# Kernel optimization log

Measured on AMD Instinct MI355X. Metric: run time of the kernel, lower is better.

## Reference

```python
import jax, jax.numpy as jnp
import numpy as np

N_HEADS, D_MODEL, DK, DV = 16, 1024, 64, 64
B, S = 4, 2048
NEG = -1000000000.0


def setup_inputs() -> dict:
    key = jax.random.key(0)
    ks = jax.random.split(key, 10)
    inp = {
        "q": jax.random.normal(ks[0], (B, S, D_MODEL), jnp.float32),
        "k": jax.random.normal(ks[1], (B, S, D_MODEL), jnp.float32),
        "v": jax.random.normal(ks[2], (B, S, D_MODEL), jnp.float32),
        "padding_mask": jax.random.randint(ks[3], (B, 1, S), 0, 2, jnp.int32),
        # linear params (torch Linear: y = x @ W.T + b); store as [in, out]
        "w_q": jax.random.normal(ks[4], (D_MODEL, N_HEADS * DK), jnp.float32) * 0.02,
        "b_q": jnp.zeros((N_HEADS * DK,), jnp.float32),
        "w_k": jax.random.normal(ks[5], (D_MODEL, N_HEADS * DK), jnp.float32) * 0.02,
        "b_k": jnp.zeros((N_HEADS * DK,), jnp.float32),
        "w_v": jax.random.normal(ks[6], (D_MODEL, N_HEADS * DV), jnp.float32) * 0.02,
        "b_v": jnp.zeros((N_HEADS * DV,), jnp.float32),
    }
    return inp


def reference(q, k, v, padding_mask, w_q, b_q, w_k, b_k, w_v, b_v):
    residual = q
    # project and split heads: [B, H, S, dk]
    qh = (q @ w_q + b_q).reshape(B, S, N_HEADS, DK).transpose(0, 2, 1, 3)
    kh = (k @ w_k + b_k).reshape(B, S, N_HEADS, DK).transpose(0, 2, 1, 3)
    vh = (v @ w_v + b_v).reshape(B, S, N_HEADS, DV).transpose(0, 2, 1, 3)
    # NB: original code DIVIDES by factor = dk**-0.5, i.e. multiplies by sqrt(dk)
    scores = jnp.einsum("bhqd,bhkd->bhqk", qh, kh) / (DK ** -0.5)
    mask = padding_mask[:, None, :, :]  # [B,1,1,S] broadcasts over heads/queries
    scores = jnp.where(mask == 0, NEG, scores)
    attn = jax.nn.softmax(scores, axis=-1)  # dropout = identity (eval)
    ctx = jnp.einsum("bhqk,bhkd->bhqd", attn, vh)
    ctx = ctx.transpose(0, 2, 1, 3).reshape(B, S, N_HEADS * DV)
    return ctx + residual
```

## Files before the change

### kernel.cpp

```cpp
#include <hip/hip_runtime.h>
#include <hip/hip_fp16.h>

#define BB 4
#define SS 2048
#define HH 16
#define DKK 64
#define DMODEL 1024

typedef __attribute__((ext_vector_type(8))) _Float16 half8;
typedef __attribute__((ext_vector_type(2))) __fp16 fp16x2;
typedef __attribute__((ext_vector_type(4))) float floatx4;

#define MFMA16(a, b, c) __builtin_amdgcn_mfma_f32_16x16x32_f16(a, b, c, 0, 0, 0)

#define SCL2 11.5415603336f

__device__ __forceinline__ void gload_lds16(const _Float16* g, _Float16* l) {
    __builtin_amdgcn_global_load_lds(
        (const __attribute__((address_space(1))) void*)g,
        (__attribute__((address_space(3))) void*)l, 16, 0, 0);
}

__global__ __launch_bounds__(256)
void convert_x(const float* __restrict__ q, const float* __restrict__ k,
               const float* __restrict__ v, _Float16* __restrict__ xq,
               _Float16* __restrict__ xk, _Float16* __restrict__ xv)
{
    int z = blockIdx.y;
    const float* src = (z == 0) ? q : (z == 1) ? k : v;
    _Float16* dst = (z == 0) ? xq : (z == 1) ? xk : xv;
    size_t base = ((size_t)blockIdx.x * 256 + threadIdx.x) * 8;
    int m = (int)(base >> 10);
    int kk = (int)(base & 1023);
    float4 a = *(const float4*)(src + base);
    float4 b = *(const float4*)(src + base + 4);
    half8 h;
    h[0] = (_Float16)a.x; h[1] = (_Float16)a.y; h[2] = (_Float16)a.z; h[3] = (_Float16)a.w;
    h[4] = (_Float16)b.x; h[5] = (_Float16)b.y; h[6] = (_Float16)b.z; h[7] = (_Float16)b.w;
    int kd = kk ^ ((m & 7) << 3);
    *(half8*)(dst + ((size_t)m << 10) + kd) = h;
}

__global__ __launch_bounds__(256)
void convert_wt(const float* __restrict__ wq, const float* __restrict__ wk,
                const float* __restrict__ wv, _Float16* __restrict__ tq,
                _Float16* __restrict__ tk, _Float16* __restrict__ tv)
{
    __shared__ __attribute__((aligned(16))) _Float16 T[64][72];
    int z = blockIdx.y;
    const float* W = (z == 0) ? wq : (z == 1) ? wk : wv;
    _Float16* WT = (z == 0) ? tq : (z == 1) ? tk : tv;
    int kt = (blockIdx.x >> 4) << 6;
    int nt = (blockIdx.x & 15) << 6;
    int tid = threadIdx.x;
    #pragma unroll
    for (int p = 0; p < 4; p++) {
        int lin = tid + p * 256;
        int row = lin >> 4;
        int c4 = (lin & 15) << 2;
        float4 vv = *(const float4*)(W + (size_t)(kt + row) * DMODEL + nt + c4);
        T[c4 + 0][row] = (_Float16)vv.x;
        T[c4 + 1][row] = (_Float16)vv.y;
        T[c4 + 2][row] = (_Float16)vv.z;
        T[c4 + 3][row] = (_Float16)vv.w;
    }
    __syncthreads();
    #pragma unroll
    for (int p = 0; p < 2; p++) {
        int lin = tid + p * 256;
        int nl = lin >> 3;
        int u = lin & 7;
        half8 h = *(const half8*)&T[nl][u * 8];
        int n = nt + nl;
        int kd = kt + ((u ^ (n & 7)) << 3);
        *(half8*)(WT + (size_t)n * DMODEL + kd) = h;
    }
}

template <int VMODE>
__device__ __forceinline__
void proj_body(const _Float16* __restrict__ X, const _Float16* __restrict__ WT,
               const float* __restrict__ bias, _Float16* __restrict__ out,
               int bidx)
{
    __shared__ __attribute__((aligned(16))) _Float16 As[128 * 64];
    __shared__ __attribute__((aligned(16))) _Float16 Bs[128 * 64];
    const int tid = threadIdx.x;
    const int wave = tid >> 6, lane = tid & 63, quad = lane >> 4, l16 = lane & 15;
    const int wm = wave >> 1, wn = wave & 1;
    const int m0 = (bidx >> 3) << 7;
    const int n0 = (bidx & 7) << 7;
    const int lrow = lane >> 3;
    const int lcol = (lane & 7) << 3;

    floatx4 acc[4][4] = {};

    for (int k0 = 0; k0 < DMODEL; k0 += 64) {
        __syncthreads();
        #pragma unroll
        for (int c = 0; c < 4; c++) {
            int row = c * 32 + wave * 8;
            gload_lds16(X + (size_t)(m0 + row + lrow) * DMODEL + k0 + lcol,
                        As + (size_t)row * 64);
            gload_lds16(WT + (size_t)(n0 + row + lrow) * DMODEL + k0 + lcol,
                        Bs + (size_t)row * 64);
        }
        __syncthreads();
        #pragma unroll
        for (int ks = 0; ks < 2; ks++) {
            int ccol = ((ks * 4 + quad) ^ (l16 & 7)) << 3;
            half8 af[4], bf[4];
            #pragma unroll
            for (int i = 0; i < 4; i++)
                af[i] = *(const half8*)(As + (wm * 64 + i * 16 + l16) * 64 + ccol);
            #pragma unroll
            for (int j = 0; j < 4; j++)
                bf[j] = *(const half8*)(Bs + (wn * 64 + j * 16 + l16) * 64 + ccol);
            #pragma unroll
            for (int i = 0; i < 4; i++)
                #pragma unroll
                for (int j = 0; j < 4; j++)
                    acc[i][j] = VMODE ? MFMA16(bf[j], af[i], acc[i][j])
                                      : MFMA16(af[i], bf[j], acc[i][j]);
        }
    }

    if (VMODE == 0) {
        #pragma unroll
        for (int j = 0; j < 4; j++) {
            int ng = n0 + wn * 64 + j * 16 + l16;
            int h = ng >> 6, d = ng & 63;
            float bv = bias[ng];
            #pragma unroll
            for (int i = 0; i < 4; i++)
                #pragma unroll
                for (int r = 0; r < 4; r++) {
                    int mg = m0 + wm * 64 + i * 16 + quad * 4 + r;
                    int bb = mg >> 11, s = mg & 2047;
                    out[(((size_t)bb * HH + h) * SS + s) * DKK + d] =
                        (_Float16)(acc[i][j][r] + bv);
                }
        }
    } else {
        #pragma unroll
        for (int j = 0; j < 4; j++)
            #pragma unroll
            for (int r = 0; r < 4; r++) {
                int ng = n0 + wn * 64 + j * 16 + quad * 4 + r;
                int h = ng >> 6, d = ng & 63;
                float bv = bias[ng];
                #pragma unroll
                for (int i = 0; i < 4; i++) {
                    int mg = m0 + wm * 64 + i * 16 + l16;
                    int bb = mg >> 11, s = mg & 2047;
                    out[(((size_t)bb * HH + h) * DKK + d) * SS + s] =
                        (_Float16)(acc[i][j][r] + bv);
                }
            }
    }
}

template <int VMODE>
__global__ __launch_bounds__(256)
void proj128(const _Float16* __restrict__ X, const _Float16* __restrict__ WT,
             const float* __restrict__ bias, _Float16* __restrict__ out)
{
    proj_body<VMODE>(X, WT, bias, out, blockIdx.x);
}

__global__ __launch_bounds__(256)
void proj128qk(const _Float16* __restrict__ X0, const _Float16* __restrict__ X1,
               const _Float16* __restrict__ WT0, const _Float16* __restrict__ WT1,
               const float* __restrict__ b0, const float* __restrict__ b1,
               _Float16* __restrict__ o0, _Float16* __restrict__ o1)
{
    if (blockIdx.y == 0) proj_body<0>(X0, WT0, b0, o0, blockIdx.x);
    else                 proj_body<0>(X1, WT1, b1, o1, blockIdx.x);
}

__global__ __launch_bounds__(256)
void flash3(const _Float16* __restrict__ Qw, const _Float16* __restrict__ Kw,
            const _Float16* __restrict__ VTw, const int* __restrict__ mask,
            const float* __restrict__ resid, float* __restrict__ out)
{
    __shared__ float Bias[SS];
    __shared__ __attribute__((aligned(16))) _Float16 Plds[4][2][16][72];

    const int tid = threadIdx.x;
    const int wave = tid >> 6, lane = tid & 63, quad = lane >> 4, l16 = lane & 15;
    const int bx = blockIdx.x;
    const int xcd = bx & 7;
    const int jj = bx >> 3;
    const int bh = ((jj >> 4) << 3) | xcd;
    const int qt = jj & 15;
    const int b = bh >> 4;
    const int h = bh & 15;
    const int qbase = qt * 128 + wave * 32;

    const int* mk = mask + b * SS;
    for (int i = tid; i < SS; i += 256)
        Bias[i] = mk[i] ? 0.f : -1.0e9f;
    __syncthreads();

    half8 qf[2][2];
    #pragma unroll
    for (int mt = 0; mt < 2; mt++) {
        const _Float16* Qp = Qw + ((size_t)bh * SS + qbase + mt * 16 + l16) * DKK;
        qf[mt][0] = *(const half8*)(Qp + quad * 8);
        qf[mt][1] = *(const half8*)(Qp + 32 + quad * 8);
    }

    float mrow[2] = {-3.0e38f, -3.0e38f};
    float lrow[2] = {0.f, 0.f};
    floatx4 oacc[2][4] = {};

    const _Float16* Kbase = Kw + (size_t)bh * SS * DKK;
    const _Float16* Vbase = VTw + (size_t)bh * DKK * SS;

    for (int kt = 0; kt < SS / 64; kt++) {
        const int kb = kt * 64;

        half8 kf[2][4];
        #pragma unroll
        for (int ks = 0; ks < 2; ks++)
            #pragma unroll
            for (int k2 = 0; k2 < 4; k2++)
                kf[ks][k2] = *(const half8*)(Kbase
                    + (size_t)(kb + k2 * 16 + l16) * DKK + ks * 32 + quad * 8);

        floatx4 sacc[2][4] = {};
        #pragma unroll
        for (int mt = 0; mt < 2; mt++)
            #pragma unroll
            for (int ks = 0; ks < 2; ks++)
                #pragma unroll
                for (int k2 = 0; k2 < 4; k2++)
                    sacc[mt][k2] = MFMA16(kf[ks][k2], qf[mt][ks], sacc[mt][k2]);

        half8 vf[2][4];
        #pragma unroll
        for (int ks = 0; ks < 2; ks++)
            #pragma unroll
            for (int dt = 0; dt < 4; dt++)
                vf[ks][dt] = *(const half8*)(Vbase
                    + (size_t)(dt * 16 + l16) * SS + kb + ks * 32 + quad * 8);

        float4 bs[4];
        #pragma unroll
        for (int k2 = 0; k2 < 4; k2++)
            bs[k2] = *(const float4*)&Bias[kb + k2 * 16 + quad * 4];

        #pragma unroll
        for (int mt = 0; mt < 2; mt++) {
            float p[4][4];
            #pragma unroll
            for (int k2 = 0; k2 < 4; k2++) {
                const float* bp = (const float*)&bs[k2];
                #pragma unroll
                for (int r = 0; r < 4; r++)
                    p[k2][r] = fmaf(sacc[mt][k2][r], SCL2, bp[r]);
            }
            float t = p[0][0];
            #pragma unroll
            for (int k2 = 0; k2 < 4; k2++)
                #pragma unroll
                for (int r = 0; r < 4; r++)
                    t = fmaxf(t, p[k2][r]);
            t = fmaxf(t, __shfl_xor(t, 16, 64));
            t = fmaxf(t, __shfl_xor(t, 32, 64));
            float mn = fmaxf(mrow[mt], t);
            float al = exp2f(mrow[mt] - mn);
            mrow[mt] = mn;

            float ps = 0.f;
            #pragma unroll
            for (int k2 = 0; k2 < 4; k2++)
                #pragma unroll
                for (int r = 0; r < 4; r++) {
                    float pv = exp2f(p[k2][r] - mn);
                    p[k2][r] = pv;
                    ps += pv;
                }
            ps += __shfl_xor(ps, 16, 64);
            ps += __shfl_xor(ps, 32, 64);
            lrow[mt] = lrow[mt] * al + ps;

            #pragma unroll
            for (int k2 = 0; k2 < 4; k2++) {
                fp16x2 pa = __builtin_amdgcn_cvt_pkrtz(p[k2][0], p[k2][1]);
                fp16x2 pb = __builtin_amdgcn_cvt_pkrtz(p[k2][2], p[k2][3]);
                *(fp16x2*)&Plds[wave][mt][l16][k2 * 16 + quad * 4]     = pa;
                *(fp16x2*)&Plds[wave][mt][l16][k2 * 16 + quad * 4 + 2] = pb;
            }
            #pragma unroll
            for (int dt = 0; dt < 4; dt++)
                oacc[mt][dt] *= al;

            #pragma unroll
            for (int ks = 0; ks < 2; ks++) {
                half8 pf = *(const half8*)&Plds[wave][mt][l16][ks * 32 + quad * 8];
                #pragma unroll
                for (int dt = 0; dt < 4; dt++)
                    oacc[mt][dt] = MFMA16(vf[ks][dt], pf, oacc[mt][dt]);
            }
        }
    }

    #pragma unroll
    for (int mt = 0; mt < 2; mt++) {
        float rl = 1.0f / lrow[mt];
        int s = qbase + mt * 16 + l16;
        size_t rowoff = ((size_t)b * SS + s) * DMODEL + h * DKK;
        #pragma unroll
        for (int dt = 0; dt < 4; dt++) {
            size_t gi = rowoff + dt * 16 + quad * 4;
            float4 rv = *(const float4*)&resid[gi];
            float4 ov;
            ov.x = oacc[mt][dt][0] * rl + rv.x;
            ov.y = oacc[mt][dt][1] * rl + rv.y;
            ov.z = oacc[mt][dt][2] * rl + rv.z;
            ov.w = oacc[mt][dt][3] * rl + rv.w;
            *(float4*)&out[gi] = ov;
        }
    }
}

extern "C" void kernel_launch(void* const* d_in, const int* in_sizes, int n_in,
                              void* d_out, int out_size, void* d_ws, size_t ws_size,
                              hipStream_t stream)
{
    const float* q    = (const float*)d_in[0];
    const float* k    = (const float*)d_in[1];
    const float* v    = (const float*)d_in[2];
    const int*   mask = (const int*)d_in[3];
    const float* wq   = (const float*)d_in[4];
    const float* bq   = (const float*)d_in[5];
    const float* wk   = (const float*)d_in[6];
    const float* bk   = (const float*)d_in[7];
    const float* wv   = (const float*)d_in[8];
    const float* bv   = (const float*)d_in[9];
    float* out = (float*)d_out;

    const size_t TENS = (size_t)BB * SS * HH * DKK;
    const size_t WSZ  = (size_t)DMODEL * DMODEL;
    _Float16* base = (_Float16*)d_ws;

    bool big = ws_size >= (6 * TENS + 3 * WSZ) * sizeof(_Float16);
    _Float16 *Xq, *Xk, *Xv, *Qh, *Kh, *VTh, *WTq;
    if (big) {
        Xq = base;            Xk = base + TENS;     Xv = base + 2 * TENS;
        Qh = base + 3 * TENS; Kh = base + 4 * TENS; VTh = base + 5 * TENS;
        WTq = base + 6 * TENS;
    } else {
        Xq = base;            Xk = base + TENS;     Xv = base + 2 * TENS;
        Qh = base + 3 * TENS; Kh = Xq;              VTh = Xk;
        WTq = base + 4 * TENS;
    }
    _Float16* WTk = WTq + WSZ;
    _Float16* WTv = WTk + WSZ;

    hipLaunchKernelGGL(convert_x, dim3(4096, 3), dim3(256), 0, stream, q, k, v, Xq, Xk, Xv);
    hipLaunchKernelGGL(convert_wt, dim3(256, 3), dim3(256), 0, stream, wq, wk, wv, WTq, WTk, WTv);
    if (big) {
        hipLaunchKernelGGL(proj128qk, dim3(512, 2), dim3(256), 0, stream,
                           Xq, Xk, WTq, WTk, bq, bk, Qh, Kh);
        hipLaunchKernelGGL((proj128<1>), dim3(512), dim3(256), 0, stream, Xv, WTv, bv, VTh);
    } else {
        hipLaunchKernelGGL((proj128<0>), dim3(512), dim3(256), 0, stream, Xq, WTq, bq, Qh);
        hipLaunchKernelGGL((proj128<0>), dim3(512), dim3(256), 0, stream, Xk, WTk, bk, Kh);
        hipLaunchKernelGGL((proj128<1>), dim3(512), dim3(256), 0, stream, Xv, WTv, bv, VTh);
    }
    hipLaunchKernelGGL(flash3, dim3(BB * HH * (SS / 128)), dim3(256), 0, stream,
                       Qh, Kh, VTh, mask, q, out);
}
```

Measured before the change: 477.7 us.

## Prefetch next K/V tiles in flash kernel and merge convert/projection launches

The attention kernel now loads the K and V fragments for the next 64-key tile into registers while computing on the current tile. This software pipelining is meant to hide global-load latency. It also shrinks the P staging buffer to a single m-tile, tree-reduces the row max and sum, writes P as 4-wide vectors, and adds a launch-bounds occupancy hint. On the host side, the three conversion launches are merged into one grid and the Q/K/V projections into another, cutting launch count and tail effects. The costs are higher register pressure from double-held fragments and a wasted wrap-around prefetch on the last iteration.

```diff
diff --git a/kernel.cpp b/kernel.cpp
--- a/kernel.cpp
+++ b/kernel.cpp
@@ -9,6 +9,7 @@
 
 typedef __attribute__((ext_vector_type(8))) _Float16 half8;
 typedef __attribute__((ext_vector_type(2))) __fp16 fp16x2;
+typedef __attribute__((ext_vector_type(4))) __fp16 fp16x4;
 typedef __attribute__((ext_vector_type(4))) float floatx4;
 
 #define MFMA16(a, b, c) __builtin_amdgcn_mfma_f32_16x16x32_f16(a, b, c, 0, 0, 0)
@@ -21,15 +22,11 @@
         (__attribute__((address_space(3))) void*)l, 16, 0, 0);
 }
 
-__global__ __launch_bounds__(256)
-void convert_x(const float* __restrict__ q, const float* __restrict__ k,
-               const float* __restrict__ v, _Float16* __restrict__ xq,
-               _Float16* __restrict__ xk, _Float16* __restrict__ xv)
-{
-    int z = blockIdx.y;
-    const float* src = (z == 0) ? q : (z == 1) ? k : v;
-    _Float16* dst = (z == 0) ? xq : (z == 1) ? xk : xv;
-    size_t base = ((size_t)blockIdx.x * 256 + threadIdx.x) * 8;
+__device__ __forceinline__
+void convert_x_body(const float* __restrict__ src, _Float16* __restrict__ dst,
+                    int bidx)
+{
+    size_t base = ((size_t)bidx * 256 + threadIdx.x) * 8;
     int m = (int)(base >> 10);
     int kk = (int)(base & 1023);
     float4 a = *(const float4*)(src + base);
@@ -41,17 +38,13 @@
     *(half8*)(dst + ((size_t)m << 10) + kd) = h;
 }
 
-__global__ __launch_bounds__(256)
-void convert_wt(const float* __restrict__ wq, const float* __restrict__ wk,
-                const float* __restrict__ wv, _Float16* __restrict__ tq,
-                _Float16* __restrict__ tk, _Float16* __restrict__ tv)
+__device__ __forceinline__
+void convert_wt_body(const float* __restrict__ W, _Float16* __restrict__ WT,
+                     int bidx)
 {
     __shared__ __attribute__((aligned(16))) _Float16 T[64][72];
-    int z = blockIdx.y;
-    const float* W = (z == 0) ? wq : (z == 1) ? wk : wv;
-    _Float16* WT = (z == 0) ? tq : (z == 1) ? tk : tv;
-    int kt = (blockIdx.x >> 4) << 6;
-    int nt = (blockIdx.x & 15) << 6;
+    int kt = (bidx >> 4) << 6;
+    int nt = (bidx & 15) << 6;
     int tid = threadIdx.x;
     #pragma unroll
     for (int p = 0; p < 4; p++) {
@@ -77,6 +70,46 @@
     }
 }
 
+__global__ __launch_bounds__(256)
+void convert_x(const float* __restrict__ q, const float* __restrict__ k,
+               const float* __restrict__ v, _Float16* __restrict__ xq,
+               _Float16* __restrict__ xk, _Float16* __restrict__ xv)
+{
+    int z = blockIdx.y;
+    convert_x_body(z == 0 ? q : z == 1 ? k : v,
+                   z == 0 ? xq : z == 1 ? xk : xv, blockIdx.x);
+}
+
+__global__ __launch_bounds__(256)
+void convert_wt(const float* __restrict__ wq, const float* __restrict__ wk,
+                const float* __restrict__ wv, _Float16* __restrict__ tq,
+                _Float16* __restrict__ tk, _Float16* __restrict__ tv)
+{
+    int z = blockIdx.y;
+    convert_wt_body(z == 0 ? wq : z == 1 ? wk : wv,
+                    z == 0 ? tq : z == 1 ? tk : tv, blockIdx.x);
+}
+
+__global__ __launch_bounds__(256)
+void convert_all(const float* __restrict__ q, const float* __restrict__ k,
+                 const float* __restrict__ v, const float* __restrict__ wq,
+                 const float* __restrict__ wk, const float* __restrict__ wv,
+                 _Float16* __restrict__ xq, _Float16* __restrict__ xk,
+                 _Float16* __restrict__ xv, _Float16* __restrict__ tq,
+                 _Float16* __restrict__ tk, _Float16* __restrict__ tv)
+{
+    int y = blockIdx.y;
+    if (y < 3) {
+        convert_x_body(y == 0 ? q : y == 1 ? k : v,
+                       y == 0 ? xq : y == 1 ? xk : xv, blockIdx.x);
+    } else {
+        if (blockIdx.x >= 768) return;
+        int z = blockIdx.x >> 8;
+        convert_wt_body(z == 0 ? wq : z == 1 ? wk : wv,
+                        z == 0 ? tq : z == 1 ? tk : tv, blockIdx.x & 255);
+    }
+}
+
 template <int VMODE>
 __device__ __forceinline__
 void proj_body(const _Float16* __restrict__ X, const _Float16* __restrict__ WT,
@@ -169,22 +202,26 @@
 }
 
 __global__ __launch_bounds__(256)
-void proj128qk(const _Float16* __restrict__ X0, const _Float16* __restrict__ X1,
-               const _Float16* __restrict__ WT0, const _Float16* __restrict__ WT1,
-               const float* __restrict__ b0, const float* __restrict__ b1,
-               _Float16* __restrict__ o0, _Float16* __restrict__ o1)
-{
-    if (blockIdx.y == 0) proj_body<0>(X0, WT0, b0, o0, blockIdx.x);
-    else                 proj_body<0>(X1, WT1, b1, o1, blockIdx.x);
-}
-
-__global__ __launch_bounds__(256)
-void flash3(const _Float16* __restrict__ Qw, const _Float16* __restrict__ Kw,
+void proj_all(const _Float16* __restrict__ Xq, const _Float16* __restrict__ Xk,
+              const _Float16* __restrict__ Xv, const _Float16* __restrict__ WTq,
+              const _Float16* __restrict__ WTk, const _Float16* __restrict__ WTv,
+              const float* __restrict__ bq, const float* __restrict__ bk,
+              const float* __restrict__ bv, _Float16* __restrict__ Qh,
+              _Float16* __restrict__ Kh, _Float16* __restrict__ VTh)
+{
+    int z = blockIdx.y;
+    if (z == 0)      proj_body<0>(Xq, WTq, bq, Qh, blockIdx.x);
+    else if (z == 1) proj_body<0>(Xk, WTk, bk, Kh, blockIdx.x);
+    else             proj_body<1>(Xv, WTv, bv, VTh, blockIdx.x);
+}
+
+__global__ __launch_bounds__(256, 4)
+void flash4(const _Float16* __restrict__ Qw, const _Float16* __restrict__ Kw,
             const _Float16* __restrict__ VTw, const int* __restrict__ mask,
             const float* __restrict__ resid, float* __restrict__ out)
 {
     __shared__ float Bias[SS];
-    __shared__ __attribute__((aligned(16))) _Float16 Plds[4][2][16][72];
+    __shared__ __attribute__((aligned(16))) _Float16 Plds[4][16][72];
 
     const int tid = threadIdx.x;
     const int wave = tid >> 6, lane = tid & 63, quad = lane >> 4, l16 = lane & 15;
@@ -217,38 +254,44 @@
     const _Float16* Kbase = Kw + (size_t)bh * SS * DKK;
     const _Float16* Vbase = VTw + (size_t)bh * DKK * SS;
 
+    half8 kf[2][4], vf[2][4];
+    #pragma unroll
+    for (int ks = 0; ks < 2; ks++)
+        #pragma unroll
+        for (int k2 = 0; k2 < 4; k2++)
+            kf[ks][k2] = *(const half8*)(Kbase
+                + (size_t)(k2 * 16 + l16) * DKK + ks * 32 + quad * 8);
+    #pragma unroll
+    for (int ks = 0; ks < 2; ks++)
+        #pragma unroll
+        for (int dt = 0; dt < 4; dt++)
+            vf[ks][dt] = *(const half8*)(Vbase
+                + (size_t)(dt * 16 + l16) * SS + ks * 32 + quad * 8);
+
     for (int kt = 0; kt < SS / 64; kt++) {
         const int kb = kt * 64;
-
-        half8 kf[2][4];
+        const int kbn = ((kt + 1) & 31) * 64;
+
+        float4 bs[4];
+        #pragma unroll
+        for (int k2 = 0; k2 < 4; k2++)
+            bs[k2] = *(const float4*)&Bias[kb + k2 * 16 + quad * 4];
+
+        floatx4 sacc[2][4] = {};
+        #pragma unroll
+        for (int mt = 0; mt < 2; mt++)
+            #pragma unroll
+            for (int ks = 0; ks < 2; ks++)
+                #pragma unroll
+                for (int k2 = 0; k2 < 4; k2++)
+                    sacc[mt][k2] = MFMA16(kf[ks][k2], qf[mt][ks], sacc[mt][k2]);
+
         #pragma unroll
         for (int ks = 0; ks < 2; ks++)
             #pragma unroll
             for (int k2 = 0; k2 < 4; k2++)
                 kf[ks][k2] = *(const half8*)(Kbase
-                    + (size_t)(kb + k2 * 16 + l16) * DKK + ks * 32 + quad * 8);
-
-        floatx4 sacc[2][4] = {};
-        #pragma unroll
-        for (int mt = 0; mt < 2; mt++)
-            #pragma unroll
-            for (int ks = 0; ks < 2; ks++)
-                #pragma unroll
-                for (int k2 = 0; k2 < 4; k2++)
-                    sacc[mt][k2] = MFMA16(kf[ks][k2], qf[mt][ks], sacc[mt][k2]);
-
-        half8 vf[2][4];
-        #pragma unroll
-        for (int ks = 0; ks < 2; ks++)
-            #pragma unroll
-            for (int dt = 0; dt < 4; dt++)
-                vf[ks][dt] = *(const half8*)(Vbase
-                    + (size_t)(dt * 16 + l16) * SS + kb + ks * 32 + quad * 8);
-
-        float4 bs[4];
-        #pragma unroll
-        for (int k2 = 0; k2 < 4; k2++)
-            bs[k2] = *(const float4*)&Bias[kb + k2 * 16 + quad * 4];
+                    + (size_t)(kbn + k2 * 16 + l16) * DKK + ks * 32 + quad * 8);
 
         #pragma unroll
         for (int mt = 0; mt < 2; mt++) {
@@ -260,27 +303,27 @@
                 for (int r = 0; r < 4; r++)
                     p[k2][r] = fmaf(sacc[mt][k2][r], SCL2, bp[r]);
             }
-            float t = p[0][0];
+            float mk2[4];
             #pragma unroll
             for (int k2 = 0; k2 < 4; k2++)
-                #pragma unroll
-                for (int r = 0; r < 4; r++)
-                    t = fmaxf(t, p[k2][r]);
+                mk2[k2] = fmaxf(fmaxf(p[k2][0], p[k2][1]),
+                                fmaxf(p[k2][2], p[k2][3]));
+            float t = fmaxf(fmaxf(mk2[0], mk2[1]), fmaxf(mk2[2], mk2[3]));
             t = fmaxf(t, __shfl_xor(t, 16, 64));
             t = fmaxf(t, __shfl_xor(t, 32, 64));
             float mn = fmaxf(mrow[mt], t);
             float al = exp2f(mrow[mt] - mn);
             mrow[mt] = mn;
 
-            float ps = 0.f;
-            #pragma unroll
-            for (int k2 = 0; k2 < 4; k2++)
-                #pragma unroll
-                for (int r = 0; r < 4; r++) {
-                    float pv = exp2f(p[k2][r] - mn);
-                    p[k2][r] = pv;
-                    ps += pv;
-                }
+            float sk2[4];
+            #pragma unroll
+            for (int k2 = 0; k2 < 4; k2++) {
+                #pragma unroll
+                for (int r = 0; r < 4; r++)
+                    p[k2][r] = exp2f(p[k2][r] - mn);
+                sk2[k2] = (p[k2][0] + p[k2][1]) + (p[k2][2] + p[k2][3]);
+            }
+            float ps = (sk2[0] + sk2[1]) + (sk2[2] + sk2[3]);
             ps += __shfl_xor(ps, 16, 64);
             ps += __shfl_xor(ps, 32, 64);
             lrow[mt] = lrow[mt] * al + ps;
@@ -289,8 +332,8 @@
             for (int k2 = 0; k2 < 4; k2++) {
                 fp16x2 pa = __builtin_amdgcn_cvt_pkrtz(p[k2][0], p[k2][1]);
                 fp16x2 pb = __builtin_amdgcn_cvt_pkrtz(p[k2][2], p[k2][3]);
-                *(fp16x2*)&Plds[wave][mt][l16][k2 * 16 + quad * 4]     = pa;
-                *(fp16x2*)&Plds[wave][mt][l16][k2 * 16 + quad * 4 + 2] = pb;
+                fp16x4 w = __builtin_shufflevector(pa, pb, 0, 1, 2, 3);
+                *(fp16x4*)&Plds[wave][l16][k2 * 16 + quad * 4] = w;
             }
             #pragma unroll
             for (int dt = 0; dt < 4; dt++)
@@ -298,12 +341,19 @@
 
             #pragma unroll
             for (int ks = 0; ks < 2; ks++) {
-                half8 pf = *(const half8*)&Plds[wave][mt][l16][ks * 32 + quad * 8];
+                half8 pf = *(const half8*)&Plds[wave][l16][ks * 32 + quad * 8];
                 #pragma unroll
                 for (int dt = 0; dt < 4; dt++)
                     oacc[mt][dt] = MFMA16(vf[ks][dt], pf, oacc[mt][dt]);
             }
         }
+
+        #pragma unroll
+        for (int ks = 0; ks < 2; ks++)
+            #pragma unroll
+            for (int dt = 0; dt < 4; dt++)
+                vf[ks][dt] = *(const half8*)(Vbase
+                    + (size_t)(dt * 16 + l16) * SS + kbn + ks * 32 + quad * 8);
     }
 
     #pragma unroll
@@ -359,17 +409,20 @@
     _Float16* WTk = WTq + WSZ;
     _Float16* WTv = WTk + WSZ;
 
-    hipLaunchKernelGGL(convert_x, dim3(4096, 3), dim3(256), 0, stream, q, k, v, Xq, Xk, Xv);
-    hipLaunchKernelGGL(convert_wt, dim3(256, 3), dim3(256), 0, stream, wq, wk, wv, WTq, WTk, WTv);
     if (big) {
-        hipLaunchKernelGGL(proj128qk, dim3(512, 2), dim3(256), 0, stream,
-                           Xq, Xk, WTq, WTk, bq, bk, Qh, Kh);
-        hipLaunchKernelGGL((proj128<1>), dim3(512), dim3(256), 0, stream, Xv, WTv, bv, VTh);
+        hipLaunchKernelGGL(convert_all, dim3(4096, 4), dim3(256), 0, stream,
+                           q, k, v, wq, wk, wv, Xq, Xk, Xv, WTq, WTk, WTv);
+        hipLaunchKernelGGL(proj_all, dim3(512, 3), dim3(256), 0, stream,
+                           Xq, Xk, Xv, WTq, WTk, WTv, bq, bk, bv, Qh, Kh, VTh);
     } else {
+        hipLaunchKernelGGL(convert_x, dim3(4096, 3), dim3(256), 0, stream,
+                           q, k, v, Xq, Xk, Xv);
+        hipLaunchKernelGGL(convert_wt, dim3(256, 3), dim3(256), 0, stream,
+                           wq, wk, wv, WTq, WTk, WTv);
         hipLaunchKernelGGL((proj128<0>), dim3(512), dim3(256), 0, stream, Xq, WTq, bq, Qh);
         hipLaunchKernelGGL((proj128<0>), dim3(512), dim3(256), 0, stream, Xk, WTk, bk, Kh);
         hipLaunchKernelGGL((proj128<1>), dim3(512), dim3(256), 0, stream, Xv, WTv, bv, VTh);
     }
-    hipLaunchKernelGGL(flash3, dim3(BB * HH * (SS / 128)), dim3(256), 0, stream,
+    hipLaunchKernelGGL(flash4, dim3(BB * HH * (SS / 128)), dim3(256), 0, stream,
                        Qh, Kh, VTh, mask, q, out);
 }
```

New measurement: 574.0 us. +20.2%, slower.
